# Kernel tuning notes

Hardware: AMD Instinct MI355X
Metric: run time of the kernel (lower is better)

The kernel has to match this reference:

```python
import jax, jax.numpy as jnp
import numpy as np

B, L, D = 32, 256, 512
D_STATE, D_CONV, EXPAND, NODE_DIM, D_FF = 16, 4, 2, 16, 2048
D_INNER = EXPAND * D
DT_RANK = D // 16


def _layernorm(x, g, b, eps=1e-5):
    mu = x.mean(-1, keepdims=True)
    var = ((x - mu) ** 2).mean(-1, keepdims=True)
    return (x - mu) * jax.lax.rsqrt(var + eps) * g + b


def _mamba(x, in_w, conv_w, conv_b, xproj_w, dt_w, dt_b, A_log, Dp, out_w):
    # Standard selective-scan (S6) Mamba inner block.
    Bb, Ll, _ = x.shape
    u, z = jnp.split(x @ in_w, 2, axis=-1)                # (B,L,d_inner) each
    pad = jnp.pad(u, ((0, 0), (D_CONV - 1, 0), (0, 0)))   # causal depthwise conv1d
    u = sum(pad[:, k:k + Ll, :] * conv_w[:, k] for k in range(D_CONV)) + conv_b
    u = jax.nn.silu(u)
    proj = u @ xproj_w                                    # (B,L,dt_rank+2*d_state)
    dt, Bm, Cm = jnp.split(proj, [DT_RANK, DT_RANK + D_STATE], axis=-1)
    dt = jax.nn.softplus(dt @ dt_w + dt_b)                # (B,L,d_inner)
    A = -jnp.exp(A_log)                                   # (d_inner,d_state)
    dA = jnp.exp(dt[..., None] * A)                       # (B,L,d_inner,d_state)
    dBu = dt[..., None] * Bm[:, :, None, :] * u[..., None]

    def step(h, inp):
        dA_t, dBu_t, C_t = inp
        h = dA_t * h + dBu_t
        return h, jnp.einsum('bds,bs->bd', h, C_t)

    h0 = jnp.zeros((Bb, D_INNER, D_STATE), x.dtype)
    _, ys = jax.lax.scan(step, h0, (dA.transpose(1, 0, 2, 3),
                                    dBu.transpose(1, 0, 2, 3),
                                    Cm.transpose(1, 0, 2)))
    y = ys.transpose(1, 0, 2) + u * Dp                    # (B,L,d_inner)
    return (y * jax.nn.silu(z)) @ out_w


def _forward(x,
             d_in_w, d_conv_w, d_conv_b, d_xproj_w, d_dt_w, d_dt_b, d_A_log, d_D, d_out_w, d_ln_g, d_ln_b,
             s_emb1, s_emb2, s_in_w, s_conv_w, s_conv_b, s_xproj_w, s_dt_w, s_dt_b, s_A_log, s_D, s_out_w, s_ln_g, s_ln_b,
             f_ln_g, f_ln_b, f_w1, f_b1, f_w2, f_b2):
    # DiffSSM: selective SSM on the first-differenced sequence, residual + LN
    xd = jnp.concatenate([x[:, :1], x[:, 1:] - x[:, :-1]], axis=1)
    x = _layernorm(x + _mamba(xd, d_in_w, d_conv_w, d_conv_b, d_xproj_w,
                              d_dt_w, d_dt_b, d_A_log, d_D, d_out_w),
                   d_ln_g, d_ln_b)
    # SpatialGraphMamba: learned adjacency over enc_in tokens, graph mix, SSM
    adj = jax.nn.softmax(jax.nn.relu(s_emb1 @ s_emb2.T), axis=-1)  # (enc_in,enc_in)
    xg = jnp.einsum('nl,bld->bnd', adj, x)
    x = _layernorm(x + _mamba(xg, s_in_w, s_conv_w, s_conv_b, s_xproj_w,
                              s_dt_w, s_dt_b, s_A_log, s_D, s_out_w),
                   s_ln_g, s_ln_b)
    # Pre-norm FFN with residual
    h = _layernorm(x, f_ln_g, f_ln_b)
    x = x + jax.nn.gelu(h @ f_w1 + f_b1) @ f_w2 + f_b2
    return x, adj


def setup_inputs() -> dict:
    key = jax.random.key(0)
    ks = iter(jax.random.split(key, 64))

    def rn(shape, s=0.02):
        return jax.random.normal(next(ks), shape, jnp.float32) * s

    A_log_init = jnp.log(jnp.broadcast_to(
        jnp.arange(1, D_STATE + 1, dtype=jnp.float32), (D_INNER, D_STATE)))
    dt_b_init = jnp.full((D_INNER,), -4.6, jnp.float32)  # softplus^-1(~0.01)

    inp = {'x': jax.random.normal(next(ks), (B, L, D), jnp.float32)}
    for p in ('d_', 's_'):
        inp[p + 'in_w'] = rn((D, 2 * D_INNER))
        inp[p + 'conv_w'] = rn((D_INNER, D_CONV), 0.1)
        inp[p + 'conv_b'] = jnp.zeros((D_INNER,), jnp.float32)
        inp[p + 'xproj_w'] = rn((D_INNER, DT_RANK + 2 * D_STATE))
        inp[p + 'dt_w'] = rn((DT_RANK, D_INNER))
        inp[p + 'dt_b'] = dt_b_init
        inp[p + 'A_log'] = A_log_init
        inp[p + 'D'] = jnp.ones((D_INNER,), jnp.float32)
        inp[p + 'out_w'] = rn((D_INNER, D))
        inp[p + 'ln_g'] = jnp.ones((D,), jnp.float32)
        inp[p + 'ln_b'] = jnp.zeros((D,), jnp.float32)
    inp['s_emb1'] = rn((L, NODE_DIM), 0.1)
    inp['s_emb2'] = rn((L, NODE_DIM), 0.1)
    inp['f_ln_g'] = jnp.ones((D,), jnp.float32)
    inp['f_ln_b'] = jnp.zeros((D,), jnp.float32)
    inp['f_w1'] = rn((D, D_FF))
    inp['f_b1'] = jnp.zeros((D_FF,), jnp.float32)
    inp['f_w2'] = rn((D_FF, D))
    inp['f_b2'] = jnp.zeros((D,), jnp.float32)
    return inp


def reference(x,
              d_in_w, d_conv_w, d_conv_b, d_xproj_w, d_dt_w, d_dt_b, d_A_log, d_D, d_out_w, d_ln_g, d_ln_b,
              s_emb1, s_emb2, s_in_w, s_conv_w, s_conv_b, s_xproj_w, s_dt_w, s_dt_b, s_A_log, s_D, s_out_w, s_ln_g, s_ln_b,
              f_ln_g, f_ln_b, f_w1, f_b1, f_w2, f_b2):
    return _forward(x,
                    d_in_w, d_conv_w, d_conv_b, d_xproj_w, d_dt_w, d_dt_b, d_A_log, d_D, d_out_w, d_ln_g, d_ln_b,
                    s_emb1, s_emb2, s_in_w, s_conv_w, s_conv_b, s_xproj_w, s_dt_w, s_dt_b, s_A_log, s_D, s_out_w, s_ln_g, s_ln_b,
                    f_ln_g, f_ln_b, f_w1, f_b1, f_w2, f_b2)
```

## Files before the change

kernel.cpp:

```cpp
#include <hip/hip_runtime.h>

#define DEV __device__ __forceinline__

typedef __bf16 bf16x8 __attribute__((ext_vector_type(8)));
typedef float  f32x4  __attribute__((ext_vector_type(4)));

DEV unsigned short f2b(float f) {
    union { float f; unsigned u; } v; v.f = f;
    unsigned r = v.u + 0x7fffu + ((v.u >> 16) & 1u);
    return (unsigned short)(r >> 16);
}
DEV float b2f(unsigned short h) {
    union { unsigned u; float f; } v; v.u = ((unsigned)h) << 16;
    return v.f;
}
DEV float sigmoidf_(float x) { return 1.f / (1.f + __expf(-x)); }
DEV float geluf_(float x) {
    float t = 0.7978845608028654f * (x + 0.044715f * x * x * x);
    return 0.5f * x * (1.f + tanhf(t));
}
DEV float softplusf_(float x) { return x > 15.f ? x : log1pf(__expf(x)); }
DEV void gload_lds16(const void* g, void* l) {
    __builtin_amdgcn_global_load_lds((const __attribute__((address_space(1))) void*)g,
                                     (__attribute__((address_space(3))) void*)l, 16, 0, 0);
}


struct WtDesc { const float* s; unsigned short* d; int K; int N; int t0; };
struct WtArgs { WtDesc m[12]; };

__global__ __launch_bounds__(256) void wtrans_k(WtArgs a) {
    __shared__ float tile[32][33];
    int t = blockIdx.x;
    int mi = 0;
#pragma unroll
    for (int j = 1; j < 12; j++) if (t >= a.m[j].t0) mi = j;
    const float* src0 = a.m[mi].s;
    unsigned short* dst0 = a.m[mi].d;
    const int K = a.m[mi].K, N = a.m[mi].N;
    const int lt = t - a.m[mi].t0;
    const int ntk = K >> 5;
    const int kt = lt % ntk, nt = lt / ntk;
    const int c = threadIdx.x & 31, r = threadIdx.x >> 5;
    const float* src = src0 + (size_t)(kt * 32) * N + nt * 32;
#pragma unroll
    for (int i = 0; i < 4; i++) tile[r + i * 8][c] = src[(size_t)(r + i * 8) * N + c];
    __syncthreads();
    unsigned short* dst = dst0 + (size_t)(nt * 32) * K + kt * 32;
#pragma unroll
    for (int i = 0; i < 4; i++) dst[(size_t)(r + i * 8) * K + c] = f2b(tile[c][r + i * 8]);
}

__global__ __launch_bounds__(256) void diff_k(const float* __restrict__ x,
                                              unsigned short* __restrict__ xd) {
    size_t idx = (size_t)blockIdx.x * 256 + threadIdx.x;
    int l = (int)((idx >> 9) & 255);
    float v = x[idx];
    if (l > 0) v -= x[idx - 512];
    xd[idx] = f2b(v);
}

__global__ __launch_bounds__(256) void adj_k(const float* __restrict__ e1,
                                             const float* __restrict__ e2,
                                             float* __restrict__ adjf,
                                             unsigned short* __restrict__ adjb) {
    const int n = blockIdx.x, tid = threadIdx.x;
    __shared__ float e1s[16];
    __shared__ float redm[4], reds[4];
    if (tid < 16) e1s[tid] = e1[n * 16 + tid];
    __syncthreads();
    const float* e2r = e2 + tid * 16;
    float dot = 0.f;
#pragma unroll
    for (int k = 0; k < 16; k++) dot = fmaf(e1s[k], e2r[k], dot);
    float v = fmaxf(dot, 0.f);
    float m = v;
#pragma unroll
    for (int o = 32; o > 0; o >>= 1) m = fmaxf(m, __shfl_xor(m, o));
    const int lane = tid & 63, wv = tid >> 6;
    if (lane == 0) redm[wv] = m;
    __syncthreads();
    m = fmaxf(fmaxf(redm[0], redm[1]), fmaxf(redm[2], redm[3]));
    float e = __expf(v - m);
    float ssum = e;
#pragma unroll
    for (int o = 32; o > 0; o >>= 1) ssum += __shfl_xor(ssum, o);
    if (lane == 0) reds[wv] = ssum;
    __syncthreads();
    ssum = reds[0] + reds[1] + reds[2] + reds[3];
    float o = e / ssum;
    adjf[(size_t)n * 256 + tid] = o;
    adjb[(size_t)n * 256 + tid] = f2b(o);
}

template<int BM, int BN, int BK, int WRN, int FM, int FN,
         int OBF, int HBIAS, int HGELU, int HRES, int HSP>
__global__ __launch_bounds__(256) void gemm_k(
    const unsigned short* __restrict__ A, const unsigned short* __restrict__ Bt,
    void* __restrict__ C, const float* __restrict__ bias, const float* __restrict__ res,
    int M, int N, int K, int lda, long sA, long sB, long sC) {
    constexpr int SMASK = BK / 8 - 1;
    constexpr int KH    = BK / 32;
    __shared__ __align__(16) unsigned short As[BM * BK];
    __shared__ __align__(16) unsigned short Bs[BN * BK];
    const int tid  = threadIdx.x;
    const int lane = tid & 63;
    const int wave = tid >> 6;
    const int wr = wave / WRN, wc = wave % WRN;
    const int bm = blockIdx.x * BM, bn = blockIdx.y * BN;
    const unsigned short* Ab = A  + (size_t)blockIdx.z * sA;
    const unsigned short* Bb = Bt + (size_t)blockIdx.z * sB;
    const int lrow  = lane & 15;
    const int klane = lane >> 4;

    f32x4 acc[FM][FN];
#pragma unroll
    for (int m = 0; m < FM; m++)
#pragma unroll
        for (int n = 0; n < FN; n++) {
            acc[m][n][0] = 0.f; acc[m][n][1] = 0.f; acc[m][n][2] = 0.f; acc[m][n][3] = 0.f;
        }

    constexpr int AI = (BM * BK) / 2048;
    constexpr int BI = (BN * BK) / 2048;

    for (int k0 = 0; k0 < K; k0 += BK) {
#pragma unroll
        for (int it = 0; it < AI; ++it) {
            int flat = (it * 256 + tid) * 8;
            int r = flat / BK, s = (flat % BK) >> 3;
            int c = (s ^ (r & SMASK)) * 8;
            gload_lds16(Ab + (size_t)(bm + r) * lda + (k0 + c),
                        &As[(it * 256 + (tid & 192)) * 8]);
        }
#pragma unroll
        for (int it = 0; it < BI; ++it) {
            int flat = (it * 256 + tid) * 8;
            int r = flat / BK, s = (flat % BK) >> 3;
            int c = (s ^ (r & SMASK)) * 8;
            gload_lds16(Bb + (size_t)(bn + r) * K + (k0 + c),
                        &Bs[(it * 256 + (tid & 192)) * 8]);
        }
        __syncthreads();
#pragma unroll
        for (int kk = 0; kk < KH; kk++) {
            bf16x8 af[FM], bfv[FN];
#pragma unroll
            for (int m = 0; m < FM; m++) {
                int rr = wr * FM * 16 + m * 16 + lrow;
                int sl = (kk * 4 + klane) ^ (rr & SMASK);
                af[m] = *(const bf16x8*)&As[rr * BK + sl * 8];
            }
#pragma unroll
            for (int n = 0; n < FN; n++) {
                int rr = wc * FN * 16 + n * 16 + lrow;
                int sl = (kk * 4 + klane) ^ (rr & SMASK);
                bfv[n] = *(const bf16x8*)&Bs[rr * BK + sl * 8];
            }
#pragma unroll
            for (int m = 0; m < FM; m++)
#pragma unroll
                for (int n = 0; n < FN; n++)
                    acc[m][n] = __builtin_amdgcn_mfma_f32_16x16x32_bf16(af[m], bfv[n], acc[m][n], 0, 0, 0);
        }
        __syncthreads();
    }

    const int r0 = (lane >> 4) << 2;
    if (OBF) {
        unsigned short* Cs = Bs;
        constexpr int PITCH = BN + 8;
        unsigned short* Cg = (unsigned short*)C;
#pragma unroll
        for (int g = 0; g < BM / 32; g++) {
            __syncthreads();
            if (wr == (g >> 1)) {
                const int mb = (g & 1) * 2;
#pragma unroll
                for (int mm = 0; mm < 2; mm++) {
#pragma unroll
                    for (int n = 0; n < FN; n++) {
                        const int cl = wc * FN * 16 + n * 16 + lrow;
                        float bv = HBIAS ? bias[bn + cl] : 0.f;
#pragma unroll
                        for (int j = 0; j < 4; j++) {
                            float v = acc[mb + mm][n][j] + bv;
                            if (HSP)   v = softplusf_(v);
                            if (HGELU) v = geluf_(v);
                            Cs[(mm * 16 + r0 + j) * PITCH + cl] = f2b(v);
                        }
                    }
                }
            }
            __syncthreads();
#pragma unroll
            for (int i = 0; i < (32 * BN) / 2048; i++) {
                int flat = (i * 256 + tid) * 8;
                int row = flat / BN, col = flat % BN;
                uint4 val = *(const uint4*)&Cs[row * PITCH + col];
                size_t oi = (size_t)blockIdx.z * sC + (size_t)(bm + g * 32 + row) * N + bn + col;
                *(uint4*)&Cg[oi] = val;
            }
        }
    } else {
#pragma unroll
        for (int n = 0; n < FN; n++) {
            const int ccol = bn + wc * FN * 16 + n * 16 + lrow;
            float bv = HBIAS ? bias[ccol] : 0.f;
#pragma unroll
            for (int m = 0; m < FM; m++) {
#pragma unroll
                for (int j = 0; j < 4; j++) {
                    const int rrow = bm + wr * FM * 16 + m * 16 + r0 + j;
                    float v = acc[m][n][j] + bv;
                    if (HSP)   v = softplusf_(v);
                    if (HGELU) v = geluf_(v);
                    if (HRES)  v += res[(size_t)rrow * N + ccol];
                    ((float*)C)[(size_t)blockIdx.z * sC + (size_t)rrow * N + ccol] = v;
                }
            }
        }
    }
}

__global__ __launch_bounds__(256) void conv_k(const unsigned short* __restrict__ uz,
                                              const float* __restrict__ w,
                                              const float* __restrict__ cb,
                                              unsigned short* __restrict__ u) {
    size_t idx = (size_t)blockIdx.x * 256 + threadIdx.x;
    int d = (int)(idx & 1023);
    size_t row = idx >> 10;
    int l = (int)(row & 255);
    float acc = cb[d];
#pragma unroll
    for (int k = 0; k < 4; k++) {
        int ls = l + k - 3;
        if (ls >= 0) {
            long rr = (long)row + k - 3;
            acc = fmaf(w[d * 4 + k], b2f(uz[((size_t)rr << 11) + d]), acc);
        }
    }
    u[idx] = f2b(acc * sigmoidf_(acc));
}

__global__ __launch_bounds__(256) void scan1_k(
    const float* __restrict__ dt,
    const unsigned short* __restrict__ u,
    const unsigned short* __restrict__ proj,
    const float* __restrict__ A_log,
    float* __restrict__ hend, float* __restrict__ Sc) {
    const int dg = blockIdx.x, c = blockIdx.y, b = blockIdx.z;
    const int d = dg * 256 + threadIdx.x;
    const size_t base = (size_t)b * 256 + c * 32;
    __shared__ float Bs[32][16];
    for (int i = threadIdx.x; i < 512; i += 256) {
        int r = i >> 4, s = i & 15;
        Bs[r][s] = b2f(proj[(base + r) * 64 + 32 + s]);
    }
    __syncthreads();
    float Aa[16];
#pragma unroll
    for (int s = 0; s < 16; s++) Aa[s] = -__expf(A_log[d * 16 + s]);
    float h[16];
#pragma unroll
    for (int s = 0; s < 16; s++) h[s] = 0.f;
    float ssum = 0.f;
    for (int l = 0; l < 32; l++) {
        size_t row = base + l;
        float dtv = dt[(row << 10) + d];
        float uu  = b2f(u[(row << 10) + d]);
        float du  = dtv * uu;
        ssum += dtv;
#pragma unroll
        for (int s = 0; s < 16; s++)
            h[s] = __expf(dtv * Aa[s]) * h[s] + du * Bs[l][s];
    }
    size_t o = (size_t)(b * 8 + c) * 1024 + d;
    Sc[o] = ssum;
#pragma unroll
    for (int s = 0; s < 16; s++) hend[o * 16 + s] = h[s];
}

__global__ __launch_bounds__(256) void scan2_k(
    const float* __restrict__ hend, const float* __restrict__ Sc,
    const float* __restrict__ A_log, float* __restrict__ hstart) {
    const int d = blockIdx.x * 256 + threadIdx.x;
    const int b = blockIdx.y;
    float Aa[16];
#pragma unroll
    for (int s = 0; s < 16; s++) Aa[s] = -__expf(A_log[d * 16 + s]);
    float h[16];
#pragma unroll
    for (int s = 0; s < 16; s++) h[s] = 0.f;
    for (int c = 0; c < 8; c++) {
        size_t o = (size_t)(b * 8 + c) * 1024 + d;
#pragma unroll
        for (int s = 0; s < 16; s++) hstart[o * 16 + s] = h[s];
        float sc = Sc[o];
#pragma unroll
        for (int s = 0; s < 16; s++)
            h[s] = __expf(sc * Aa[s]) * h[s] + hend[o * 16 + s];
    }
}

__global__ __launch_bounds__(256) void scan3_k(
    const float* __restrict__ dt,
    const unsigned short* __restrict__ u,
    const unsigned short* __restrict__ uz,
    const unsigned short* __restrict__ proj,
    const float* __restrict__ A_log,
    const float* __restrict__ Dp,
    const float* __restrict__ hstart,
    unsigned short* __restrict__ yg) {
    const int dg = blockIdx.x, c = blockIdx.y, b = blockIdx.z;
    const int d = dg * 256 + threadIdx.x;
    const size_t base = (size_t)b * 256 + c * 32;
    __shared__ float BCs[32][32];
    for (int i = threadIdx.x; i < 1024; i += 256) {
        int r = i >> 5, s = i & 31;
        BCs[r][s] = b2f(proj[(base + r) * 64 + 32 + s]);
    }
    __syncthreads();
    float Aa[16];
#pragma unroll
    for (int s = 0; s < 16; s++) Aa[s] = -__expf(A_log[d * 16 + s]);
    const float Dd = Dp[d];
    float h[16];
    size_t ho = ((size_t)(b * 8 + c) * 1024 + d) * 16;
#pragma unroll
    for (int s = 0; s < 16; s++) h[s] = hstart[ho + s];
    for (int l = 0; l < 32; l++) {
        size_t row = base + l;
        float dtv = dt[(row << 10) + d];
        float uu  = b2f(u[(row << 10) + d]);
        float zz  = b2f(uz[(row << 11) + 1024 + d]);
        float du  = dtv * uu;
        float y = 0.f;
#pragma unroll
        for (int s = 0; s < 16; s++) {
            h[s] = __expf(dtv * Aa[s]) * h[s] + du * BCs[l][s];
            y = fmaf(h[s], BCs[l][16 + s], y);
        }
        y = fmaf(uu, Dd, y);
        yg[(row << 10) + d] = f2b(y * (zz * sigmoidf_(zz)));
    }
}

template<int HRES, int OF32, int OBF>
__global__ __launch_bounds__(256) void ln_k(const float* __restrict__ xin,
                                            const float* __restrict__ resin,
                                            const float* __restrict__ g,
                                            const float* __restrict__ b,
                                            float* __restrict__ outf,
                                            unsigned short* __restrict__ outb) {
    const int row = blockIdx.x, tid = threadIdx.x;
    float2 v = ((const float2*)(xin + (size_t)row * 512))[tid];
    if (HRES) {
        float2 r2 = ((const float2*)(resin + (size_t)row * 512))[tid];
        v.x += r2.x; v.y += r2.y;
    }
    float s = v.x + v.y, q = v.x * v.x + v.y * v.y;
#pragma unroll
    for (int o = 32; o > 0; o >>= 1) { s += __shfl_xor(s, o); q += __shfl_xor(q, o); }
    __shared__ float sm[4], qm[4];
    const int lane = tid & 63, wv = tid >> 6;
    if (lane == 0) { sm[wv] = s; qm[wv] = q; }
    __syncthreads();
    s = sm[0] + sm[1] + sm[2] + sm[3];
    q = qm[0] + qm[1] + qm[2] + qm[3];
    const float mu = s * (1.f / 512.f);
    const float ri = rsqrtf(q * (1.f / 512.f) - mu * mu + 1e-5f);
    float2 gg = ((const float2*)g)[tid];
    float2 bb = ((const float2*)b)[tid];
    float o0 = (v.x - mu) * ri * gg.x + bb.x;
    float o1 = (v.y - mu) * ri * gg.y + bb.y;
    if (OF32) ((float2*)(outf + (size_t)row * 512))[tid] = make_float2(o0, o1);
    if (OBF) {
        unsigned short* ob = outb + (size_t)row * 512 + tid * 2;
        ob[0] = f2b(o0); ob[1] = f2b(o1);
    }
}

__global__ __launch_bounds__(256) void trans_k(const float* __restrict__ x1,
                                               unsigned short* __restrict__ xt) {
    __shared__ float tile[32][33];
    const int b = blockIdx.z;
    const int d0 = blockIdx.x * 32, l0 = blockIdx.y * 32;
    const int c = threadIdx.x & 31, r = threadIdx.x >> 5;
    const float* src = x1 + ((size_t)b * 256 + l0) * 512 + d0;
#pragma unroll
    for (int i = 0; i < 4; i++) tile[r + i * 8][c] = src[(size_t)(r + i * 8) * 512 + c];
    __syncthreads();
    unsigned short* dst = xt + ((size_t)b * 512 + d0) * 256 + l0;
#pragma unroll
    for (int i = 0; i < 4; i++) dst[(size_t)(r + i * 8) * 256 + c] = f2b(tile[c][r + i * 8]);
}

constexpr size_t OFF_WT_DIN  = 0;
constexpr size_t OFF_WT_SIN  = OFF_WT_DIN  + 2048ull * 512 * 2;
constexpr size_t OFF_WT_DOUT = OFF_WT_SIN  + 2048ull * 512 * 2;
constexpr size_t OFF_WT_SOUT = OFF_WT_DOUT + 512ull * 1024 * 2;
constexpr size_t OFF_WT_F1   = OFF_WT_SOUT + 512ull * 1024 * 2;
constexpr size_t OFF_WT_F2   = OFF_WT_F1   + 2048ull * 512 * 2;
constexpr size_t OFF_XPT_D   = OFF_WT_F2   + 512ull * 2048 * 2;
constexpr size_t OFF_XPT_S   = OFF_XPT_D   + 64ull * 1024 * 2;
constexpr size_t OFF_DTT_D   = OFF_XPT_S   + 64ull * 1024 * 2;
constexpr size_t OFF_DTT_S   = OFF_DTT_D   + 1024ull * 32 * 2;
constexpr size_t OFF_ACT     = OFF_DTT_S   + 1024ull * 32 * 2;
constexpr size_t OFF_UZ      = OFF_ACT  + 8192ull * 512 * 2;
constexpr size_t OFF_U       = OFF_UZ   + 8192ull * 2048 * 2;
constexpr size_t OFF_PROJ    = OFF_U    + 8192ull * 1024 * 2;
constexpr size_t OFF_YG      = OFF_PROJ + 8192ull * 64 * 2;
constexpr size_t OFF_MOUT    = OFF_YG   + 8192ull * 1024 * 2;
constexpr size_t OFF_X1      = OFF_MOUT + 8192ull * 512 * 4;
constexpr size_t OFF_X2      = OFF_X1   + 8192ull * 512 * 4;
constexpr size_t OFF_X1T     = OFF_X2   + 8192ull * 512 * 4;
constexpr size_t OFF_ADJB    = OFF_X1T  + 32ull * 512 * 256 * 2;
constexpr size_t OFF_DT      = OFF_ADJB + 256ull * 256 * 2;
constexpr size_t OFF_HST     = OFF_DT   + 8192ull * 1024 * 4;
constexpr size_t OFF_SC      = OFF_HST  + 32ull * 8 * 1024 * 16 * 4;

extern "C" void kernel_launch(void* const* d_in, const int* in_sizes, int n_in,
                              void* d_out, int out_size, void* d_ws, size_t ws_size,
                              hipStream_t stream) {
    (void)in_sizes; (void)n_in; (void)out_size; (void)ws_size;
    const float* x      = (const float*)d_in[0];
    const float* dinw   = (const float*)d_in[1];
    const float* dconvw = (const float*)d_in[2];
    const float* dconvb = (const float*)d_in[3];
    const float* dxproj = (const float*)d_in[4];
    const float* ddtw   = (const float*)d_in[5];
    const float* ddtb   = (const float*)d_in[6];
    const float* dAlog  = (const float*)d_in[7];
    const float* dD     = (const float*)d_in[8];
    const float* doutw  = (const float*)d_in[9];
    const float* dlng   = (const float*)d_in[10];
    const float* dlnb   = (const float*)d_in[11];
    const float* sinw   = (const float*)d_in[12];
    const float* sconvw = (const float*)d_in[13];
    const float* sconvb = (const float*)d_in[14];
    const float* sxproj = (const float*)d_in[15];
    const float* sdtw   = (const float*)d_in[16];
    const float* sdtb   = (const float*)d_in[17];
    const float* sAlog  = (const float*)d_in[18];
    const float* sD     = (const float*)d_in[19];
    const float* soutw  = (const float*)d_in[20];
    const float* slng   = (const float*)d_in[21];
    const float* slnb   = (const float*)d_in[22];
    const float* semb1  = (const float*)d_in[23];
    const float* semb2  = (const float*)d_in[24];
    const float* flng   = (const float*)d_in[25];
    const float* flnb   = (const float*)d_in[26];
    const float* fw1    = (const float*)d_in[27];
    const float* fb1    = (const float*)d_in[28];
    const float* fw2    = (const float*)d_in[29];
    const float* fb2    = (const float*)d_in[30];

    char* ws = (char*)d_ws;
    unsigned short* wtDin  = (unsigned short*)(ws + OFF_WT_DIN);
    unsigned short* wtSin  = (unsigned short*)(ws + OFF_WT_SIN);
    unsigned short* wtDout = (unsigned short*)(ws + OFF_WT_DOUT);
    unsigned short* wtSout = (unsigned short*)(ws + OFF_WT_SOUT);
    unsigned short* wtF1   = (unsigned short*)(ws + OFF_WT_F1);
    unsigned short* wtF2   = (unsigned short*)(ws + OFF_WT_F2);
    unsigned short* xptD   = (unsigned short*)(ws + OFF_XPT_D);
    unsigned short* xptS   = (unsigned short*)(ws + OFF_XPT_S);
    unsigned short* dttD   = (unsigned short*)(ws + OFF_DTT_D);
    unsigned short* dttS   = (unsigned short*)(ws + OFF_DTT_S);
    unsigned short* actIn  = (unsigned short*)(ws + OFF_ACT);
    unsigned short* uzBuf  = (unsigned short*)(ws + OFF_UZ);
    unsigned short* uBuf   = (unsigned short*)(ws + OFF_U);
    unsigned short* projB  = (unsigned short*)(ws + OFF_PROJ);
    unsigned short* ygBuf  = (unsigned short*)(ws + OFF_YG);
    float*          moutB  = (float*)(ws + OFF_MOUT);
    float*          hendB  = moutB;
    float*          x1Buf  = (float*)(ws + OFF_X1);
    float*          x2Buf  = (float*)(ws + OFF_X2);
    unsigned short* x1tBuf = (unsigned short*)(ws + OFF_X1T);
    unsigned short* adjB   = (unsigned short*)(ws + OFF_ADJB);
    float*          dtBuf  = (float*)(ws + OFF_DT);
    float*          hstB   = (float*)(ws + OFF_HST);
    float*          scB    = (float*)(ws + OFF_SC);
    unsigned short* hBuf   = uBuf;
    unsigned short* midBuf = uzBuf;

    float* outX   = (float*)d_out;
    float* outAdj = outX + 4194304;

    WtArgs wa;
    wa.m[0]  = WtDesc{dinw,   wtDin,  512,  2048, 0};
    wa.m[1]  = WtDesc{sinw,   wtSin,  512,  2048, 1024};
    wa.m[2]  = WtDesc{doutw,  wtDout, 1024, 512,  2048};
    wa.m[3]  = WtDesc{soutw,  wtSout, 1024, 512,  2560};
    wa.m[4]  = WtDesc{fw1,    wtF1,   512,  2048, 3072};
    wa.m[5]  = WtDesc{fw2,    wtF2,   2048, 512,  4096};
    wa.m[6]  = WtDesc{dxproj, xptD,   1024, 64,   5120};
    wa.m[7]  = WtDesc{sxproj, xptS,   1024, 64,   5184};
    wa.m[8]  = WtDesc{ddtw,   dttD,   32,   1024, 5248};
    wa.m[9]  = WtDesc{sdtw,   dttS,   32,   1024, 5280};
    wa.m[10] = WtDesc{dinw,   wtDin,  512,  2048, 0x7fffffff};
    wa.m[11] = WtDesc{dinw,   wtDin,  512,  2048, 0x7fffffff};
    wtrans_k<<<dim3(5312), dim3(256), 0, stream>>>(wa);

    diff_k<<<dim3(16384), dim3(256), 0, stream>>>(x, actIn);
    adj_k<<<dim3(256), dim3(256), 0, stream>>>(semb1, semb2, outAdj, adjB);

    gemm_k<128,128,64,2,4,4, 1,0,0,0,0><<<dim3(64,16,1), dim3(256), 0, stream>>>(
        actIn, wtDin, uzBuf, nullptr, nullptr, 8192, 2048, 512, 512, 0, 0, 0);
    conv_k<<<dim3(32768), dim3(256), 0, stream>>>(uzBuf, dconvw, dconvb, uBuf);
    gemm_k<128,64,64,2,4,2, 1,0,0,0,0><<<dim3(64,1,1), dim3(256), 0, stream>>>(
        uBuf, xptD, projB, nullptr, nullptr, 8192, 64, 1024, 1024, 0, 0, 0);
    gemm_k<128,128,32,2,4,4, 0,1,0,0,1><<<dim3(64,8,1), dim3(256), 0, stream>>>(
        projB, dttD, dtBuf, ddtb, nullptr, 8192, 1024, 32, 64, 0, 0, 0);
    scan1_k<<<dim3(4,8,32), dim3(256), 0, stream>>>(dtBuf, uBuf, projB, dAlog, hendB, scB);
    scan2_k<<<dim3(4,32),   dim3(256), 0, stream>>>(hendB, scB, dAlog, hstB);
    scan3_k<<<dim3(4,8,32), dim3(256), 0, stream>>>(dtBuf, uBuf, uzBuf, projB, dAlog, dD, hstB, ygBuf);
    gemm_k<128,128,64,2,4,4, 0,0,0,0,0><<<dim3(64,4,1), dim3(256), 0, stream>>>(
        ygBuf, wtDout, moutB, nullptr, nullptr, 8192, 512, 1024, 1024, 0, 0, 0);
    ln_k<1,1,0><<<dim3(8192), dim3(256), 0, stream>>>(moutB, x, dlng, dlnb, x1Buf, nullptr);

    trans_k<<<dim3(16,8,32), dim3(256), 0, stream>>>(x1Buf, x1tBuf);
    gemm_k<128,128,64,2,4,4, 1,0,0,0,0><<<dim3(2,4,32), dim3(256), 0, stream>>>(
        adjB, x1tBuf, actIn, nullptr, nullptr, 256, 512, 256, 256, 0, 131072, 131072);
    gemm_k<128,128,64,2,4,4, 1,0,0,0,0><<<dim3(64,16,1), dim3(256), 0, stream>>>(
        actIn, wtSin, uzBuf, nullptr, nullptr, 8192, 2048, 512, 512, 0, 0, 0);
    conv_k<<<dim3(32768), dim3(256), 0, stream>>>(uzBuf, sconvw, sconvb, uBuf);
    gemm_k<128,64,64,2,4,2, 1,0,0,0,0><<<dim3(64,1,1), dim3(256), 0, stream>>>(
        uBuf, xptS, projB, nullptr, nullptr, 8192, 64, 1024, 1024, 0, 0, 0);
    gemm_k<128,128,32,2,4,4, 0,1,0,0,1><<<dim3(64,8,1), dim3(256), 0, stream>>>(
        projB, dttS, dtBuf, sdtb, nullptr, 8192, 1024, 32, 64, 0, 0, 0);
    scan1_k<<<dim3(4,8,32), dim3(256), 0, stream>>>(dtBuf, uBuf, projB, sAlog, hendB, scB);
    scan2_k<<<dim3(4,32),   dim3(256), 0, stream>>>(hendB, scB, sAlog, hstB);
    scan3_k<<<dim3(4,8,32), dim3(256), 0, stream>>>(dtBuf, uBuf, uzBuf, projB, sAlog, sD, hstB, ygBuf);
    gemm_k<128,128,64,2,4,4, 0,0,0,0,0><<<dim3(64,4,1), dim3(256), 0, stream>>>(
        ygBuf, wtSout, moutB, nullptr, nullptr, 8192, 512, 1024, 1024, 0, 0, 0);
    ln_k<1,1,0><<<dim3(8192), dim3(256), 0, stream>>>(moutB, x1Buf, slng, slnb, x2Buf, nullptr);

    ln_k<0,0,1><<<dim3(8192), dim3(256), 0, stream>>>(x2Buf, nullptr, flng, flnb, nullptr, hBuf);
    gemm_k<128,128,64,2,4,4, 1,1,1,0,0><<<dim3(64,16,1), dim3(256), 0, stream>>>(
        hBuf, wtF1, midBuf, fb1, nullptr, 8192, 2048, 512, 512, 0, 0, 0);
    gemm_k<128,128,64,2,4,4, 0,1,0,1,0><<<dim3(64,4,1), dim3(256), 0, stream>>>(
        midBuf, wtF2, outX, fb2, x2Buf, 8192, 512, 2048, 2048, 0, 0, 0);
}
```

Baseline: 613.4 us.

## Double-buffer GEMM LDS tiles, vectorize diff/conv kernels, shrink x-proj tiles

The GEMM kernel gets two LDS buffers so the async global-to-LDS load of the next K tile is issued before the MFMAs on the current tile, and the per-iteration sync pattern changes to match. The diff and depthwise conv kernels now handle 4 and 8 elements per thread with float4 and uint4 loads and stores instead of scalar accesses. The skinny x-projection GEMM (N=64) switches to 64x64 tiles, doubling its block count to improve occupancy. Double buffering doubles the LDS footprint, which may reduce blocks per CU for the larger tile configurations.

```diff
diff --git a/kernel.cpp b/kernel.cpp
--- a/kernel.cpp
+++ b/kernel.cpp
@@ -53,11 +53,16 @@
 
 __global__ __launch_bounds__(256) void diff_k(const float* __restrict__ x,
                                               unsigned short* __restrict__ xd) {
-    size_t idx = (size_t)blockIdx.x * 256 + threadIdx.x;
+    size_t i4 = (size_t)blockIdx.x * 256 + threadIdx.x;
+    size_t idx = i4 * 4;
     int l = (int)((idx >> 9) & 255);
-    float v = x[idx];
-    if (l > 0) v -= x[idx - 512];
-    xd[idx] = f2b(v);
+    float4 v = *(const float4*)&x[idx];
+    if (l > 0) {
+        float4 p = *(const float4*)&x[idx - 512];
+        v.x -= p.x; v.y -= p.y; v.z -= p.z; v.w -= p.w;
+    }
+    unsigned short o[4] = {f2b(v.x), f2b(v.y), f2b(v.z), f2b(v.w)};
+    *(unsigned long long*)&xd[idx] = *(unsigned long long*)o;
 }
 
 __global__ __launch_bounds__(256) void adj_k(const float* __restrict__ e1,
@@ -101,8 +106,10 @@
     int M, int N, int K, int lda, long sA, long sB, long sC) {
     constexpr int SMASK = BK / 8 - 1;
     constexpr int KH    = BK / 32;
-    __shared__ __align__(16) unsigned short As[BM * BK];
-    __shared__ __align__(16) unsigned short Bs[BN * BK];
+    constexpr int AI = (BM * BK) / 2048;
+    constexpr int BI = (BN * BK) / 2048;
+    __shared__ __align__(16) unsigned short As[2][BM * BK];
+    __shared__ __align__(16) unsigned short Bs[2][BN * BK];
     const int tid  = threadIdx.x;
     const int lane = tid & 63;
     const int wave = tid >> 6;
@@ -121,17 +128,14 @@
             acc[m][n][0] = 0.f; acc[m][n][1] = 0.f; acc[m][n][2] = 0.f; acc[m][n][3] = 0.f;
         }
 
-    constexpr int AI = (BM * BK) / 2048;
-    constexpr int BI = (BN * BK) / 2048;
-
-    for (int k0 = 0; k0 < K; k0 += BK) {
+    auto STAGE = [&](int buf, int k0) {
 #pragma unroll
         for (int it = 0; it < AI; ++it) {
             int flat = (it * 256 + tid) * 8;
             int r = flat / BK, s = (flat % BK) >> 3;
             int c = (s ^ (r & SMASK)) * 8;
             gload_lds16(Ab + (size_t)(bm + r) * lda + (k0 + c),
-                        &As[(it * 256 + (tid & 192)) * 8]);
+                        &As[buf][(it * 256 + (tid & 192)) * 8]);
         }
 #pragma unroll
         for (int it = 0; it < BI; ++it) {
@@ -139,9 +143,10 @@
             int r = flat / BK, s = (flat % BK) >> 3;
             int c = (s ^ (r & SMASK)) * 8;
             gload_lds16(Bb + (size_t)(bn + r) * K + (k0 + c),
-                        &Bs[(it * 256 + (tid & 192)) * 8]);
-        }
-        __syncthreads();
+                        &Bs[buf][(it * 256 + (tid & 192)) * 8]);
+        }
+    };
+    auto COMPUTE = [&](int buf) {
 #pragma unroll
         for (int kk = 0; kk < KH; kk++) {
             bf16x8 af[FM], bfv[FN];
@@ -149,13 +154,13 @@
             for (int m = 0; m < FM; m++) {
                 int rr = wr * FM * 16 + m * 16 + lrow;
                 int sl = (kk * 4 + klane) ^ (rr & SMASK);
-                af[m] = *(const bf16x8*)&As[rr * BK + sl * 8];
+                af[m] = *(const bf16x8*)&As[buf][rr * BK + sl * 8];
             }
 #pragma unroll
             for (int n = 0; n < FN; n++) {
                 int rr = wc * FN * 16 + n * 16 + lrow;
                 int sl = (kk * 4 + klane) ^ (rr & SMASK);
-                bfv[n] = *(const bf16x8*)&Bs[rr * BK + sl * 8];
+                bfv[n] = *(const bf16x8*)&Bs[buf][rr * BK + sl * 8];
             }
 #pragma unroll
             for (int m = 0; m < FM; m++)
@@ -163,19 +168,32 @@
                 for (int n = 0; n < FN; n++)
                     acc[m][n] = __builtin_amdgcn_mfma_f32_16x16x32_bf16(af[m], bfv[n], acc[m][n], 0, 0, 0);
         }
+    };
+
+    const int nt = K / BK;
+    STAGE(0, 0);
+    __syncthreads();
+    for (int t = 0; t < nt; t += 2) {
+        if (t + 1 < nt) STAGE(1, (t + 1) * BK);
+        COMPUTE(0);
         __syncthreads();
+        if (t + 1 < nt) {
+            if (t + 2 < nt) STAGE(0, (t + 2) * BK);
+            COMPUTE(1);
+            if (t + 2 < nt) __syncthreads();
+        }
     }
 
     const int r0 = (lane >> 4) << 2;
     if (OBF) {
-        unsigned short* Cs = Bs;
+        unsigned short* Cs = Bs[0];
         constexpr int PITCH = BN + 8;
         unsigned short* Cg = (unsigned short*)C;
 #pragma unroll
         for (int g = 0; g < BM / 32; g++) {
             __syncthreads();
-            if (wr == (g >> 1)) {
-                const int mb = (g & 1) * 2;
+            if (wr == (g * 2) / FM) {
+                const int mb = (g * 2) % FM;
 #pragma unroll
                 for (int mm = 0; mm < 2; mm++) {
 #pragma unroll
@@ -227,20 +245,33 @@
                                               const float* __restrict__ w,
                                               const float* __restrict__ cb,
                                               unsigned short* __restrict__ u) {
-    size_t idx = (size_t)blockIdx.x * 256 + threadIdx.x;
-    int d = (int)(idx & 1023);
-    size_t row = idx >> 10;
+    int t = blockIdx.x * 256 + threadIdx.x;
+    int dg = t & 127;
+    size_t row = (size_t)(t >> 7);
     int l = (int)(row & 255);
-    float acc = cb[d];
+    int d0 = dg * 8;
+    float acc[8];
+#pragma unroll
+    for (int j = 0; j < 8; j++) acc[j] = cb[d0 + j];
 #pragma unroll
     for (int k = 0; k < 4; k++) {
         int ls = l + k - 3;
         if (ls >= 0) {
-            long rr = (long)row + k - 3;
-            acc = fmaf(w[d * 4 + k], b2f(uz[((size_t)rr << 11) + d]), acc);
-        }
-    }
-    u[idx] = f2b(acc * sigmoidf_(acc));
+            const unsigned short* src = uz + (((size_t)row + k - 3) << 11) + d0;
+            uint4 v = *(const uint4*)src;
+            const unsigned short* vs = (const unsigned short*)&v;
+#pragma unroll
+            for (int j = 0; j < 8; j++)
+                acc[j] = fmaf(w[(d0 + j) * 4 + k], b2f(vs[j]), acc[j]);
+        }
+    }
+    unsigned short o[8];
+#pragma unroll
+    for (int j = 0; j < 8; j++) {
+        float a = acc[j];
+        o[j] = f2b(a * sigmoidf_(a));
+    }
+    *(uint4*)(u + (row << 10) + d0) = *(const uint4*)o;
 }
 
 __global__ __launch_bounds__(256) void scan1_k(
@@ -502,13 +533,13 @@
     wa.m[11] = WtDesc{dinw,   wtDin,  512,  2048, 0x7fffffff};
     wtrans_k<<<dim3(5312), dim3(256), 0, stream>>>(wa);
 
-    diff_k<<<dim3(16384), dim3(256), 0, stream>>>(x, actIn);
+    diff_k<<<dim3(4096), dim3(256), 0, stream>>>(x, actIn);
     adj_k<<<dim3(256), dim3(256), 0, stream>>>(semb1, semb2, outAdj, adjB);
 
     gemm_k<128,128,64,2,4,4, 1,0,0,0,0><<<dim3(64,16,1), dim3(256), 0, stream>>>(
         actIn, wtDin, uzBuf, nullptr, nullptr, 8192, 2048, 512, 512, 0, 0, 0);
-    conv_k<<<dim3(32768), dim3(256), 0, stream>>>(uzBuf, dconvw, dconvb, uBuf);
-    gemm_k<128,64,64,2,4,2, 1,0,0,0,0><<<dim3(64,1,1), dim3(256), 0, stream>>>(
+    conv_k<<<dim3(4096), dim3(256), 0, stream>>>(uzBuf, dconvw, dconvb, uBuf);
+    gemm_k<64,64,64,2,2,2, 1,0,0,0,0><<<dim3(128,1,1), dim3(256), 0, stream>>>(
         uBuf, xptD, projB, nullptr, nullptr, 8192, 64, 1024, 1024, 0, 0, 0);
     gemm_k<128,128,32,2,4,4, 0,1,0,0,1><<<dim3(64,8,1), dim3(256), 0, stream>>>(
         projB, dttD, dtBuf, ddtb, nullptr, 8192, 1024, 32, 64, 0, 0, 0);
@@ -524,8 +555,8 @@
         adjB, x1tBuf, actIn, nullptr, nullptr, 256, 512, 256, 256, 0, 131072, 131072);
     gemm_k<128,128,64,2,4,4, 1,0,0,0,0><<<dim3(64,16,1), dim3(256), 0, stream>>>(
         actIn, wtSin, uzBuf, nullptr, nullptr, 8192, 2048, 512, 512, 0, 0, 0);
-    conv_k<<<dim3(32768), dim3(256), 0, stream>>>(uzBuf, sconvw, sconvb, uBuf);
-    gemm_k<128,64,64,2,4,2, 1,0,0,0,0><<<dim3(64,1,1), dim3(256), 0, stream>>>(
+    conv_k<<<dim3(4096), dim3(256), 0, stream>>>(uzBuf, sconvw, sconvb, uBuf);
+    gemm_k<64,64,64,2,2,2, 1,0,0,0,0><<<dim3(128,1,1), dim3(256), 0, stream>>>(
         uBuf, xptS, projB, nullptr, nullptr, 8192, 64, 1024, 1024, 0, 0, 0);
     gemm_k<128,128,32,2,4,4, 0,1,0,0,1><<<dim3(64,8,1), dim3(256), 0, stream>>>(
         projB, dttS, dtBuf, sdtb, nullptr, 8192, 1024, 32, 64, 0, 0, 0);
```

Result: slower. 653.2 us (+6.5%).
